# Optimization experiments

Hardware: AMD Instinct MI355X
Metric: run time of the kernel (lower is better)

## Reference

```python
import jax, jax.numpy as jnp
import numpy as np

N, E, G, D, C = 100000, 1600000, 128, 64, 10  # nodes, edges, graphs, feat dim, classes


def setup_inputs() -> dict:
    key = jax.random.key(0)
    ks = jax.random.split(key, 14)
    s = 0.05
    return {
        "x": jax.random.normal(ks[0], (N, D), jnp.float32),
        # edge update MLP: concat(h_src,h_dst) -> hidden -> message (dim D to allow u_mul_e)
        "We1": jax.random.normal(ks[1], (2 * D, D), jnp.float32) * s,
        "be1": jnp.zeros((D,), jnp.float32),
        "We2": jax.random.normal(ks[2], (D, D), jnp.float32) * s,
        "be2": jnp.zeros((D,), jnp.float32),
        # node update MLP (hidden_dim -> hidden_dim)
        "Wn": jax.random.normal(ks[3], (D, D), jnp.float32) * s,
        "bn": jnp.zeros((D,), jnp.float32),
        # attention-pooling gate Linear(hidden_dim, 1)
        "Wg": jax.random.normal(ks[4], (D, 1), jnp.float32) * s,
        "bg": jnp.zeros((1,), jnp.float32),
        # final classifier
        "Wfc": jax.random.normal(ks[5], (D, C), jnp.float32) * s,
        "bfc": jnp.zeros((C,), jnp.float32),
        # graph structure
        "src": jax.random.randint(ks[6], (E,), 0, N),
        "dst": jax.random.randint(ks[7], (E,), 0, N),
        "graph_ids": jnp.sort(jax.random.randint(ks[8], (N,), 0, G)),
    }


def reference(x, We1, be1, We2, be2, Wn, bn, Wg, bg, Wfc, bfc, src, dst, graph_ids):
    h = x  # [N, D]
    # apply_edges: edge MLP on (h_src, h_dst) -> message m per edge  [E, D]
    e_in = jnp.concatenate([h[src], h[dst]], axis=-1)  # [E, 2D]
    m = jax.nn.relu(e_in @ We1 + be1) @ We2 + be2
    # update_all: u_mul_e('h','m') then sum-reduce onto destination nodes
    h_neigh = jax.ops.segment_sum(h[src] * m, dst, num_segments=N)  # [N, D]
    # apply_nodes: node MLP
    h2 = jax.nn.relu(h_neigh @ Wn + bn)  # [N, D]
    # GlobalAttentionPooling: per-graph softmax over node gates, weighted sum
    gate = h2 @ Wg + bg  # [N, 1]
    gmax = jax.ops.segment_max(gate, graph_ids, num_segments=G)  # [G, 1]
    a = jnp.exp(gate - gmax[graph_ids])
    denom = jax.ops.segment_sum(a, graph_ids, num_segments=G)  # [G, 1]
    a = a / denom[graph_ids]
    pooled = jax.ops.segment_sum(a * h2, graph_ids, num_segments=G)  # [G, D]
    return pooled @ Wfc + bfc  # [G, C]
```

## Files before the change

kernel.cpp:

```cpp
#include <hip/hip_runtime.h>
#include <hip/hip_bf16.h>

#define D 64
#define BSH 6
#define BNODES 64
#define NBMAX 2048
#define EB 4096

typedef _Float16 f16;
typedef _Float16 f16x4 __attribute__((ext_vector_type(4)));
typedef _Float16 f16x8 __attribute__((ext_vector_type(8)));
typedef float f32x4 __attribute__((ext_vector_type(4)));

__device__ __forceinline__ int sw7(int m, int k) {
    return (m << 7) + (((k >> 3) ^ (m & 7)) << 3) + (k & 7);
}
__device__ __forceinline__ int sw6(int m, int k) {
    return (m << 6) + ((((k >> 3) ^ (m & 7)) & 7) << 3) + (k & 7);
}

__global__ __launch_bounds__(256) void bucket_hist(
    const int* __restrict__ dst, int* __restrict__ bhist, int E, int NB)
{
    __shared__ int lhist[NBMAX];
    int tid = threadIdx.x;
    for (int b = tid; b < NB; b += 256) lhist[b] = 0;
    __syncthreads();
    int base = blockIdx.x * EB;
#pragma unroll
    for (int r = 0; r < EB / 256; ++r) {
        int e = base + r * 256 + tid;
        if (e < E) atomicAdd(&lhist[dst[e] >> BSH], 1);
    }
    __syncthreads();
    for (int b = tid; b < NB; b += 256) {
        int v = lhist[b];
        if (v) atomicAdd(&bhist[b], v);
    }
}

__global__ __launch_bounds__(256) void bucket_scan(
    const int* __restrict__ bhist, int* __restrict__ boff,
    int* __restrict__ bcursor, int NB)
{
    __shared__ int lds[256];
    int tid = threadIdx.x;
    int chunk = (NB + 255) / 256;
    int b0 = tid * chunk;
    int b1 = min(b0 + chunk, NB);
    int s = 0;
    for (int b = b0; b < b1; ++b) s += bhist[b];
    lds[tid] = s;
    __syncthreads();
    for (int d2 = 1; d2 < 256; d2 <<= 1) {
        int v = (tid >= d2) ? lds[tid - d2] : 0;
        __syncthreads();
        lds[tid] += v;
        __syncthreads();
    }
    int run = (tid == 0) ? 0 : lds[tid - 1];
    for (int b = b0; b < b1; ++b) {
        boff[b] = run;
        bcursor[b] = run;
        run += bhist[b];
    }
    if (tid == 255) boff[NB] = lds[255];
}

__global__ __launch_bounds__(256) void bucket_fill(
    const int* __restrict__ dst, const int* __restrict__ src,
    int* __restrict__ bcursor, int2* __restrict__ eix, int E, int NB)
{
    __shared__ int lhist[NBMAX];
    __shared__ int lcur[NBMAX];
    int tid = threadIdx.x;
    for (int b = tid; b < NB; b += 256) lhist[b] = 0;
    __syncthreads();
    int base = blockIdx.x * EB;
    int dv[EB / 256];
#pragma unroll
    for (int r = 0; r < EB / 256; ++r) {
        int e = base + r * 256 + tid;
        dv[r] = (e < E) ? dst[e] : -1;
        if (dv[r] >= 0) atomicAdd(&lhist[dv[r] >> BSH], 1);
    }
    __syncthreads();
    for (int b = tid; b < NB; b += 256) {
        int v = lhist[b];
        lcur[b] = v ? atomicAdd(&bcursor[b], v) : 0;
    }
    __syncthreads();
#pragma unroll
    for (int r = 0; r < EB / 256; ++r) {
        int e = base + r * 256 + tid;
        if (dv[r] >= 0) {
            int p = atomicAdd(&lcur[dv[r] >> BSH], 1);
            eix[p] = make_int2(src[e], dv[r]);
        }
    }
}

__global__ __launch_bounds__(256) void bucket_sort(
    const int2* __restrict__ eix, const int* __restrict__ boff,
    int2* __restrict__ eix2, int NB)
{
    __shared__ int h64[BNODES];
    __shared__ int cur64[BNODES];
    int bk = blockIdx.x;
    int s = boff[bk], e = boff[bk + 1];
    int tid = threadIdx.x;
    int nbase = bk << BSH;

    if (tid < BNODES) h64[tid] = 0;
    __syncthreads();
    for (int i = s + tid; i < e; i += 256)
        atomicAdd(&h64[eix[i].y - nbase], 1);
    __syncthreads();
    if (tid < BNODES) {
        int v = h64[tid];
        int inc = v;
        for (int d2 = 1; d2 < BNODES; d2 <<= 1) {
            int t = __shfl_up(inc, d2);
            if (tid >= d2) inc += t;
        }
        cur64[tid] = inc - v;
    }
    __syncthreads();
    for (int i = s + tid; i < e; i += 256) {
        int2 ed = eix[i];
        int slot = atomicAdd(&cur64[ed.y - nbase], 1);
        eix2[s + slot] = ed;
    }
}

__global__ __launch_bounds__(256, 2) void edge_mfma_kernel(
    const float* __restrict__ x,
    const float* __restrict__ We1, const float* __restrict__ be1,
    const float* __restrict__ We2, const float* __restrict__ be2,
    const int2* __restrict__ eix,
    float* __restrict__ hneigh, int N, int E, int T)
{
    __shared__ __attribute__((aligned(16))) float XCs[4][16 * 68];
    __shared__ __attribute__((aligned(16))) f16   Hbs[4][16 * 64];
    __shared__ int edsts[4][16];

    const int tid  = threadIdx.x;
    const int w    = tid >> 6;
    const int lane = tid & 63;
    const int l15  = lane & 15;
    const int quad = lane >> 4;

    float* XC  = XCs[w];
    f16*   Hb  = Hbs[w];
    int*   edst = edsts[w];

    f16x8 wb1[4][4];
#pragma unroll
    for (int kt = 0; kt < 4; ++kt)
#pragma unroll
        for (int nf = 0; nf < 4; ++nf) {
            int n = nf * 16 + l15;
#pragma unroll
            for (int j = 0; j < 8; ++j)
                wb1[kt][nf][j] = (f16)We1[(kt * 32 + quad * 8 + j) * 64 + n];
        }
    f16x8 wb2[2][4];
#pragma unroll
    for (int kt = 0; kt < 2; ++kt)
#pragma unroll
        for (int nf = 0; nf < 4; ++nf) {
            int n = nf * 16 + l15;
#pragma unroll
            for (int j = 0; j < 8; ++j)
                wb2[kt][nf][j] = (f16)We2[(kt * 32 + quad * 8 + j) * 64 + n];
        }

    float b1v[4], b2v[4];
#pragma unroll
    for (int nf = 0; nf < 4; ++nf) {
        b1v[nf] = be1[nf * 16 + l15];
        b2v[nf] = be2[nf * 16 + l15];
    }

    const int wid = blockIdx.x * 4 + w;
    const int nw  = gridDim.x * 4;

    for (int tile = wid; tile < T; tile += nw) {
        const int e0 = tile * 16;

        int2 pe = eix[min(e0 + l15, E - 1)];
        const float* ps = x + (size_t)pe.x * D;
        const float* pd = x + (size_t)pe.y * D;
        float4 s0 = *(const float4*)(ps + quad * 8);
        float4 s1 = *(const float4*)(ps + quad * 8 + 4);
        float4 s2 = *(const float4*)(ps + 32 + quad * 8);
        float4 s3 = *(const float4*)(ps + 32 + quad * 8 + 4);
        float4 d0v = *(const float4*)(pd + quad * 8);
        float4 d1v = *(const float4*)(pd + quad * 8 + 4);
        float4 d2v = *(const float4*)(pd + 32 + quad * 8);
        float4 d3v = *(const float4*)(pd + 32 + quad * 8 + 4);

        int prevD = (e0 > 0)      ? eix[e0 - 1].y  : -2;
        int nextD = (e0 + 16 < E) ? eix[e0 + 16].y : -2;

        *(float4*)&XC[l15 * 68 + quad * 8]          = s0;
        *(float4*)&XC[l15 * 68 + quad * 8 + 4]      = s1;
        *(float4*)&XC[l15 * 68 + 32 + quad * 8]     = s2;
        *(float4*)&XC[l15 * 68 + 32 + quad * 8 + 4] = s3;
        if (quad == 0) edst[l15] = (e0 + l15 < E) ? pe.y : N;

        f16x8 ah[4];
        ah[0][0]=(f16)s0.x; ah[0][1]=(f16)s0.y; ah[0][2]=(f16)s0.z; ah[0][3]=(f16)s0.w;
        ah[0][4]=(f16)s1.x; ah[0][5]=(f16)s1.y; ah[0][6]=(f16)s1.z; ah[0][7]=(f16)s1.w;
        ah[1][0]=(f16)s2.x; ah[1][1]=(f16)s2.y; ah[1][2]=(f16)s2.z; ah[1][3]=(f16)s2.w;
        ah[1][4]=(f16)s3.x; ah[1][5]=(f16)s3.y; ah[1][6]=(f16)s3.z; ah[1][7]=(f16)s3.w;
        ah[2][0]=(f16)d0v.x; ah[2][1]=(f16)d0v.y; ah[2][2]=(f16)d0v.z; ah[2][3]=(f16)d0v.w;
        ah[2][4]=(f16)d1v.x; ah[2][5]=(f16)d1v.y; ah[2][6]=(f16)d1v.z; ah[2][7]=(f16)d1v.w;
        ah[3][0]=(f16)d2v.x; ah[3][1]=(f16)d2v.y; ah[3][2]=(f16)d2v.z; ah[3][3]=(f16)d2v.w;
        ah[3][4]=(f16)d3v.x; ah[3][5]=(f16)d3v.y; ah[3][6]=(f16)d3v.z; ah[3][7]=(f16)d3v.w;

        f32x4 acc[4] = {{0.f,0.f,0.f,0.f},{0.f,0.f,0.f,0.f},
                        {0.f,0.f,0.f,0.f},{0.f,0.f,0.f,0.f}};
#pragma unroll
        for (int kt = 0; kt < 4; ++kt)
#pragma unroll
            for (int nf = 0; nf < 4; ++nf)
                acc[nf] = __builtin_amdgcn_mfma_f32_16x16x32_f16(
                    ah[kt], wb1[kt][nf], acc[nf], 0, 0, 0);

#pragma unroll
        for (int nf = 0; nf < 4; ++nf)
#pragma unroll
            for (int i2 = 0; i2 < 4; ++i2)
                Hb[sw6(quad * 4 + i2, nf * 16 + l15)] =
                    (f16)fmaxf(acc[nf][i2] + b1v[nf], 0.f);

        f32x4 dd[4] = {{0.f,0.f,0.f,0.f},{0.f,0.f,0.f,0.f},
                       {0.f,0.f,0.f,0.f},{0.f,0.f,0.f,0.f}};
#pragma unroll
        for (int kt = 0; kt < 2; ++kt) {
            f16x8 ah2 = *(const f16x8*)&Hb[sw6(l15, kt * 32 + quad * 8)];
#pragma unroll
            for (int nf = 0; nf < 4; ++nf)
                dd[nf] = __builtin_amdgcn_mfma_f32_16x16x32_f16(
                    ah2, wb2[kt][nf], dd[nf], 0, 0, 0);
        }

#pragma unroll
        for (int nf = 0; nf < 4; ++nf)
#pragma unroll
            for (int i2 = 0; i2 < 4; ++i2) {
                int a = (quad * 4 + i2) * 68 + nf * 16 + l15;
                XC[a] = (dd[nf][i2] + b2v[nf]) * XC[a];
            }

        {
            int j = lane;
            float a = 0.f;
            int cur = edst[0];
            int runStart = 0;
#pragma unroll
            for (int ii = 0; ii < 16; ++ii) {
                a += XC[ii * 68 + j];
                int nxt = (ii < 15) ? edst[ii + 1] : -3;
                if (nxt != cur) {
                    bool firstRun = (runStart == 0);
                    bool lastRun = (ii == 15) || (nxt >= N);
                    bool complete = (!firstRun || prevD != cur) &&
                                    (!lastRun || nextD != cur);
                    if (complete) hneigh[(size_t)cur * D + j] = a;
                    else atomicAdd(&hneigh[(size_t)cur * D + j], a);
                    a = 0.f; cur = nxt; runStart = ii + 1;
                }
            }
        }
    }
}

__global__ __launch_bounds__(256, 4) void node_mfma_kernel(
    float* __restrict__ h,
    const float* __restrict__ Wn, const float* __restrict__ bn,
    const float* __restrict__ Wg, const float* __restrict__ bg,
    float* __restrict__ gate, int N, int T)
{
    __shared__ __attribute__((aligned(16))) f16 ANhi[64 * 64];
    __shared__ __attribute__((aligned(16))) f16 ANlo[64 * 64];

    const int tid = threadIdx.x;
    const int w = tid >> 6;
    const int lane = tid & 63;
    const int l15 = lane & 15;
    const int quad = lane >> 4;
    const int m0 = w * 16;

    f16x8 wn[2][4];
#pragma unroll
    for (int kt = 0; kt < 2; ++kt)
#pragma unroll
        for (int nf = 0; nf < 4; ++nf) {
            int n = nf * 16 + l15;
#pragma unroll
            for (int j = 0; j < 8; ++j)
                wn[kt][nf][j] = (f16)Wn[(kt * 32 + quad * 8 + j) * 64 + n];
        }

    float bnv[4], wgv[4];
#pragma unroll
    for (int nt = 0; nt < 4; ++nt) {
        bnv[nt] = bn[nt * 16 + l15];
        wgv[nt] = Wg[nt * 16 + l15];
    }
    const float bgv = bg[0];

    for (int tile = blockIdx.x; tile < T; tile += gridDim.x) {
        const int t0 = tile * 64;

        {
            int i = tid >> 2;
            int q = tid & 3;
            int node = min(t0 + i, N - 1);
            const float* p = h + (size_t)node * D + q * 16;
#pragma unroll
            for (int r = 0; r < 4; ++r) {
                float4 v = *(const float4*)(p + r * 4);
                int k = q * 16 + r * 4;
                f16x4 hv, lv;
                hv[0] = (f16)v.x; lv[0] = (f16)(v.x - (float)hv[0]);
                hv[1] = (f16)v.y; lv[1] = (f16)(v.y - (float)hv[1]);
                hv[2] = (f16)v.z; lv[2] = (f16)(v.z - (float)hv[2]);
                hv[3] = (f16)v.w; lv[3] = (f16)(v.w - (float)hv[3]);
                *(f16x4*)&ANhi[sw6(i, k)] = hv;
                *(f16x4*)&ANlo[sw6(i, k)] = lv;
            }
        }
        __syncthreads();

        f32x4 cacc[4] = {{0.f,0.f,0.f,0.f},{0.f,0.f,0.f,0.f},{0.f,0.f,0.f,0.f},{0.f,0.f,0.f,0.f}};
#pragma unroll
        for (int kt = 0; kt < 2; ++kt) {
            int k = kt * 32 + quad * 8;
            f16x8 ah = *(const f16x8*)&ANhi[sw6(m0 + l15, k)];
            f16x8 al = *(const f16x8*)&ANlo[sw6(m0 + l15, k)];
#pragma unroll
            for (int nf = 0; nf < 4; ++nf) {
                cacc[nf] = __builtin_amdgcn_mfma_f32_16x16x32_f16(ah, wn[kt][nf], cacc[nf], 0, 0, 0);
                cacc[nf] = __builtin_amdgcn_mfma_f32_16x16x32_f16(al, wn[kt][nf], cacc[nf], 0, 0, 0);
            }
        }
        __syncthreads();

        float gpart[4] = {0.f, 0.f, 0.f, 0.f};
#pragma unroll
        for (int nt = 0; nt < 4; ++nt) {
            int n = nt * 16 + l15;
#pragma unroll
            for (int i2 = 0; i2 < 4; ++i2) {
                int m = t0 + m0 + quad * 4 + i2;
                float v = fmaxf(cacc[nt][i2] + bnv[nt], 0.f);
                if (m < N) h[(size_t)m * D + n] = v;
                gpart[i2] += v * wgv[nt];
            }
        }
#pragma unroll
        for (int s = 1; s < 16; s <<= 1) {
#pragma unroll
            for (int i2 = 0; i2 < 4; ++i2) gpart[i2] += __shfl_xor(gpart[i2], s);
        }
        if (l15 == 0) {
#pragma unroll
            for (int i2 = 0; i2 < 4; ++i2) {
                int m = t0 + m0 + quad * 4 + i2;
                if (m < N) gate[m] = gpart[i2] + bgv;
            }
        }
    }
}

__global__ __launch_bounds__(256) void pool_kernel(
    const float* __restrict__ h2,
    const float* __restrict__ gate,
    const int* __restrict__ gid,
    const float* __restrict__ Wfc, const float* __restrict__ bfc,
    float* __restrict__ out, int N, int C)
{
    int g = blockIdx.x;
    int tid = threadIdx.x;

    int lo = 0, hi = N;
    while (lo < hi) { int mid = (lo + hi) >> 1; if (gid[mid] < g) lo = mid + 1; else hi = mid; }
    int s = lo;
    hi = N;
    while (lo < hi) { int mid = (lo + hi) >> 1; if (gid[mid] < g + 1) lo = mid + 1; else hi = mid; }
    int e = lo;

    __shared__ float red[256];
    __shared__ float accs[4][D];
    __shared__ float dens[4];

    float m = -INFINITY;
    for (int i = s + tid; i < e; i += 256) m = fmaxf(m, gate[i]);
    red[tid] = m;
    __syncthreads();
    for (int w = 128; w > 0; w >>= 1) {
        if (tid < w) red[tid] = fmaxf(red[tid], red[tid + w]);
        __syncthreads();
    }
    float gmax = red[0];
    __syncthreads();

    int f = tid & (D - 1);
    int grp = tid >> 6;
    float acc = 0.0f, den = 0.0f;
    for (int i = s + grp; i < e; i += 4) {
        float w = expf(gate[i] - gmax);
        acc += w * h2[(size_t)i * D + f];
        if (f == 0) den += w;
    }
    accs[grp][f] = acc;
    if (f == 0) dens[grp] = den;
    __syncthreads();

    if (tid < D) {
        float p = accs[0][tid] + accs[1][tid] + accs[2][tid] + accs[3][tid];
        float dn = dens[0] + dens[1] + dens[2] + dens[3];
        p = (e > s) ? (p / dn) : 0.0f;
        red[tid] = p;
    }
    __syncthreads();

    if (tid < C) {
        float o = bfc[tid];
#pragma unroll
        for (int k = 0; k < D; ++k) o += red[k] * Wfc[k * C + tid];
        out[g * C + tid] = o;
    }
}

extern "C" void kernel_launch(void* const* d_in, const int* in_sizes, int n_in,
                              void* d_out, int out_size, void* d_ws, size_t ws_size,
                              hipStream_t stream) {
    const float* x   = (const float*)d_in[0];
    const float* We1 = (const float*)d_in[1];
    const float* be1 = (const float*)d_in[2];
    const float* We2 = (const float*)d_in[3];
    const float* be2 = (const float*)d_in[4];
    const float* Wn  = (const float*)d_in[5];
    const float* bn  = (const float*)d_in[6];
    const float* Wg  = (const float*)d_in[7];
    const float* bg  = (const float*)d_in[8];
    const float* Wfc = (const float*)d_in[9];
    const float* bfc = (const float*)d_in[10];
    const int* src = (const int*)d_in[11];
    const int* dst = (const int*)d_in[12];
    const int* gid = (const int*)d_in[13];

    const int N = in_sizes[0] / D;
    const int E = in_sizes[11];
    const int C = 10;
    const int G = out_size / C;
    const int NB = (N + BNODES - 1) / BNODES;

    int2*  eix2   = (int2*)d_ws;
    int2*  eixA   = eix2 + E;
    float* hneigh = (float*)eixA;
    float* gate   = hneigh + (size_t)(N + 1) * D;
    int*   bhist  = (int*)(gate + N);
    int*   boff   = bhist + NB;
    int*   bcursor= boff + NB + 1;
    float* outp   = (float*)d_out;

    const int Bh = (E + EB - 1) / EB;
    const int Te = (E + 15) / 16;
    const int Tn = (N + 63) / 64;

    hipMemsetAsync(bhist, 0, (size_t)NB * sizeof(int), stream);

    bucket_hist<<<Bh, 256, 0, stream>>>(dst, bhist, E, NB);
    bucket_scan<<<1, 256, 0, stream>>>(bhist, boff, bcursor, NB);
    bucket_fill<<<Bh, 256, 0, stream>>>(dst, src, bcursor, eixA, E, NB);
    bucket_sort<<<NB, 256, 0, stream>>>(eixA, boff, eix2, NB);

    hipMemsetAsync(hneigh, 0, (size_t)(N + 1) * D * sizeof(float), stream);

    edge_mfma_kernel<<<512, 256, 0, stream>>>(x, We1, be1, We2, be2,
                                              eix2, hneigh, N, E, Te);
    node_mfma_kernel<<<1024, 256, 0, stream>>>(hneigh, Wn, bn, Wg, bg, gate, N, Tn);
    pool_kernel<<<G, 256, 0, stream>>>(hneigh, gate, gid, Wfc, bfc, outp, N, C);
}
```

Baseline: 391.2 us.

## Process two 16-edge subtiles per wave and prefetch next tile's edge indices

Each wave in the edge kernel now handles 32 edges per iteration as two interleaved 16-row MFMA subtiles, doubling the independent gathers and MFMA chains in flight. The edge index pairs for the next tile are loaded one iteration ahead to hide the dependent index-to-feature load latency. Segment reduction runs over 32 rows, so fewer partial runs hit atomics at tile boundaries. This raises register and LDS use per wave, which can reduce occupancy under the 2-blocks-per-CU launch bound.

```diff
diff --git a/kernel.cpp b/kernel.cpp
--- a/kernel.cpp
+++ b/kernel.cpp
@@ -12,9 +12,6 @@
 typedef _Float16 f16x8 __attribute__((ext_vector_type(8)));
 typedef float f32x4 __attribute__((ext_vector_type(4)));
 
-__device__ __forceinline__ int sw7(int m, int k) {
-    return (m << 7) + (((k >> 3) ^ (m & 7)) << 3) + (k & 7);
-}
 __device__ __forceinline__ int sw6(int m, int k) {
     return (m << 6) + ((((k >> 3) ^ (m & 7)) & 7) << 3) + (k & 7);
 }
@@ -140,9 +137,9 @@
     const int2* __restrict__ eix,
     float* __restrict__ hneigh, int N, int E, int T)
 {
-    __shared__ __attribute__((aligned(16))) float XCs[4][16 * 68];
-    __shared__ __attribute__((aligned(16))) f16   Hbs[4][16 * 64];
-    __shared__ int edsts[4][16];
+    __shared__ __attribute__((aligned(16))) float XCs[4][32 * 68];
+    __shared__ __attribute__((aligned(16))) f16   Hbs[4][32 * 64];
+    __shared__ int edsts[4][32];
 
     const int tid  = threadIdx.x;
     const int w    = tid >> 6;
@@ -185,73 +182,120 @@
     const int wid = blockIdx.x * 4 + w;
     const int nw  = gridDim.x * 4;
 
+    int2 peA = eix[min(wid * 32 + l15, E - 1)];
+    int2 peB = eix[min(wid * 32 + 16 + l15, E - 1)];
+
     for (int tile = wid; tile < T; tile += nw) {
-        const int e0 = tile * 16;
-
-        int2 pe = eix[min(e0 + l15, E - 1)];
-        const float* ps = x + (size_t)pe.x * D;
-        const float* pd = x + (size_t)pe.y * D;
-        float4 s0 = *(const float4*)(ps + quad * 8);
-        float4 s1 = *(const float4*)(ps + quad * 8 + 4);
-        float4 s2 = *(const float4*)(ps + 32 + quad * 8);
-        float4 s3 = *(const float4*)(ps + 32 + quad * 8 + 4);
-        float4 d0v = *(const float4*)(pd + quad * 8);
-        float4 d1v = *(const float4*)(pd + quad * 8 + 4);
-        float4 d2v = *(const float4*)(pd + 32 + quad * 8);
-        float4 d3v = *(const float4*)(pd + 32 + quad * 8 + 4);
+        const int e0 = tile * 32;
+
+        const float* psA = x + (size_t)peA.x * D;
+        const float* pdA = x + (size_t)peA.y * D;
+        const float* psB = x + (size_t)peB.x * D;
+        const float* pdB = x + (size_t)peB.y * D;
+        float4 sA0 = *(const float4*)(psA + quad * 8);
+        float4 sA1 = *(const float4*)(psA + quad * 8 + 4);
+        float4 sA2 = *(const float4*)(psA + 32 + quad * 8);
+        float4 sA3 = *(const float4*)(psA + 32 + quad * 8 + 4);
+        float4 dA0 = *(const float4*)(pdA + quad * 8);
+        float4 dA1 = *(const float4*)(pdA + quad * 8 + 4);
+        float4 dA2 = *(const float4*)(pdA + 32 + quad * 8);
+        float4 dA3 = *(const float4*)(pdA + 32 + quad * 8 + 4);
+        float4 sB0 = *(const float4*)(psB + quad * 8);
+        float4 sB1 = *(const float4*)(psB + quad * 8 + 4);
+        float4 sB2 = *(const float4*)(psB + 32 + quad * 8);
+        float4 sB3 = *(const float4*)(psB + 32 + quad * 8 + 4);
+        float4 dB0 = *(const float4*)(pdB + quad * 8);
+        float4 dB1 = *(const float4*)(pdB + quad * 8 + 4);
+        float4 dB2 = *(const float4*)(pdB + 32 + quad * 8);
+        float4 dB3 = *(const float4*)(pdB + 32 + quad * 8 + 4);
+
+        int tn = tile + nw;
+        int2 peA_n = eix[min(tn * 32 + l15, E - 1)];
+        int2 peB_n = eix[min(tn * 32 + 16 + l15, E - 1)];
 
         int prevD = (e0 > 0)      ? eix[e0 - 1].y  : -2;
-        int nextD = (e0 + 16 < E) ? eix[e0 + 16].y : -2;
-
-        *(float4*)&XC[l15 * 68 + quad * 8]          = s0;
-        *(float4*)&XC[l15 * 68 + quad * 8 + 4]      = s1;
-        *(float4*)&XC[l15 * 68 + 32 + quad * 8]     = s2;
-        *(float4*)&XC[l15 * 68 + 32 + quad * 8 + 4] = s3;
-        if (quad == 0) edst[l15] = (e0 + l15 < E) ? pe.y : N;
-
-        f16x8 ah[4];
-        ah[0][0]=(f16)s0.x; ah[0][1]=(f16)s0.y; ah[0][2]=(f16)s0.z; ah[0][3]=(f16)s0.w;
-        ah[0][4]=(f16)s1.x; ah[0][5]=(f16)s1.y; ah[0][6]=(f16)s1.z; ah[0][7]=(f16)s1.w;
-        ah[1][0]=(f16)s2.x; ah[1][1]=(f16)s2.y; ah[1][2]=(f16)s2.z; ah[1][3]=(f16)s2.w;
-        ah[1][4]=(f16)s3.x; ah[1][5]=(f16)s3.y; ah[1][6]=(f16)s3.z; ah[1][7]=(f16)s3.w;
-        ah[2][0]=(f16)d0v.x; ah[2][1]=(f16)d0v.y; ah[2][2]=(f16)d0v.z; ah[2][3]=(f16)d0v.w;
-        ah[2][4]=(f16)d1v.x; ah[2][5]=(f16)d1v.y; ah[2][6]=(f16)d1v.z; ah[2][7]=(f16)d1v.w;
-        ah[3][0]=(f16)d2v.x; ah[3][1]=(f16)d2v.y; ah[3][2]=(f16)d2v.z; ah[3][3]=(f16)d2v.w;
-        ah[3][4]=(f16)d3v.x; ah[3][5]=(f16)d3v.y; ah[3][6]=(f16)d3v.z; ah[3][7]=(f16)d3v.w;
-
-        f32x4 acc[4] = {{0.f,0.f,0.f,0.f},{0.f,0.f,0.f,0.f},
+        int nextD = (e0 + 32 < E) ? eix[e0 + 32].y : -2;
+
+        *(float4*)&XC[l15 * 68 + quad * 8]               = sA0;
+        *(float4*)&XC[l15 * 68 + quad * 8 + 4]           = sA1;
+        *(float4*)&XC[l15 * 68 + 32 + quad * 8]          = sA2;
+        *(float4*)&XC[l15 * 68 + 32 + quad * 8 + 4]      = sA3;
+        *(float4*)&XC[(16 + l15) * 68 + quad * 8]          = sB0;
+        *(float4*)&XC[(16 + l15) * 68 + quad * 8 + 4]      = sB1;
+        *(float4*)&XC[(16 + l15) * 68 + 32 + quad * 8]     = sB2;
+        *(float4*)&XC[(16 + l15) * 68 + 32 + quad * 8 + 4] = sB3;
+        if (quad == 0) {
+            edst[l15]      = (e0 + l15 < E)      ? peA.y : N;
+            edst[16 + l15] = (e0 + 16 + l15 < E) ? peB.y : N;
+        }
+
+        f16x8 ahA[4], ahB[4];
+        ahA[0][0]=(f16)sA0.x; ahA[0][1]=(f16)sA0.y; ahA[0][2]=(f16)sA0.z; ahA[0][3]=(f16)sA0.w;
+        ahA[0][4]=(f16)sA1.x; ahA[0][5]=(f16)sA1.y; ahA[0][6]=(f16)sA1.z; ahA[0][7]=(f16)sA1.w;
+        ahA[1][0]=(f16)sA2.x; ahA[1][1]=(f16)sA2.y; ahA[1][2]=(f16)sA2.z; ahA[1][3]=(f16)sA2.w;
+        ahA[1][4]=(f16)sA3.x; ahA[1][5]=(f16)sA3.y; ahA[1][6]=(f16)sA3.z; ahA[1][7]=(f16)sA3.w;
+        ahA[2][0]=(f16)dA0.x; ahA[2][1]=(f16)dA0.y; ahA[2][2]=(f16)dA0.z; ahA[2][3]=(f16)dA0.w;
+        ahA[2][4]=(f16)dA1.x; ahA[2][5]=(f16)dA1.y; ahA[2][6]=(f16)dA1.z; ahA[2][7]=(f16)dA1.w;
+        ahA[3][0]=(f16)dA2.x; ahA[3][1]=(f16)dA2.y; ahA[3][2]=(f16)dA2.z; ahA[3][3]=(f16)dA2.w;
+        ahA[3][4]=(f16)dA3.x; ahA[3][5]=(f16)dA3.y; ahA[3][6]=(f16)dA3.z; ahA[3][7]=(f16)dA3.w;
+        ahB[0][0]=(f16)sB0.x; ahB[0][1]=(f16)sB0.y; ahB[0][2]=(f16)sB0.z; ahB[0][3]=(f16)sB0.w;
+        ahB[0][4]=(f16)sB1.x; ahB[0][5]=(f16)sB1.y; ahB[0][6]=(f16)sB1.z; ahB[0][7]=(f16)sB1.w;
+        ahB[1][0]=(f16)sB2.x; ahB[1][1]=(f16)sB2.y; ahB[1][2]=(f16)sB2.z; ahB[1][3]=(f16)sB2.w;
+        ahB[1][4]=(f16)sB3.x; ahB[1][5]=(f16)sB3.y; ahB[1][6]=(f16)sB3.z; ahB[1][7]=(f16)sB3.w;
+        ahB[2][0]=(f16)dB0.x; ahB[2][1]=(f16)dB0.y; ahB[2][2]=(f16)dB0.z; ahB[2][3]=(f16)dB0.w;
+        ahB[2][4]=(f16)dB1.x; ahB[2][5]=(f16)dB1.y; ahB[2][6]=(f16)dB1.z; ahB[2][7]=(f16)dB1.w;
+        ahB[3][0]=(f16)dB2.x; ahB[3][1]=(f16)dB2.y; ahB[3][2]=(f16)dB2.z; ahB[3][3]=(f16)dB2.w;
+        ahB[3][4]=(f16)dB3.x; ahB[3][5]=(f16)dB3.y; ahB[3][6]=(f16)dB3.z; ahB[3][7]=(f16)dB3.w;
+
+        f32x4 accA[4] = {{0.f,0.f,0.f,0.f},{0.f,0.f,0.f,0.f},
+                         {0.f,0.f,0.f,0.f},{0.f,0.f,0.f,0.f}};
+        f32x4 accB[4] = {{0.f,0.f,0.f,0.f},{0.f,0.f,0.f,0.f},
+                         {0.f,0.f,0.f,0.f},{0.f,0.f,0.f,0.f}};
+#pragma unroll
+        for (int kt = 0; kt < 4; ++kt)
+#pragma unroll
+            for (int nf = 0; nf < 4; ++nf) {
+                accA[nf] = __builtin_amdgcn_mfma_f32_16x16x32_f16(
+                    ahA[kt], wb1[kt][nf], accA[nf], 0, 0, 0);
+                accB[nf] = __builtin_amdgcn_mfma_f32_16x16x32_f16(
+                    ahB[kt], wb1[kt][nf], accB[nf], 0, 0, 0);
+            }
+
+#pragma unroll
+        for (int nf = 0; nf < 4; ++nf)
+#pragma unroll
+            for (int i2 = 0; i2 < 4; ++i2) {
+                Hb[sw6(quad * 4 + i2, nf * 16 + l15)] =
+                    (f16)fmaxf(accA[nf][i2] + b1v[nf], 0.f);
+                Hb[sw6(16 + quad * 4 + i2, nf * 16 + l15)] =
+                    (f16)fmaxf(accB[nf][i2] + b1v[nf], 0.f);
+            }
+
+        f32x4 ddA[4] = {{0.f,0.f,0.f,0.f},{0.f,0.f,0.f,0.f},
                         {0.f,0.f,0.f,0.f},{0.f,0.f,0.f,0.f}};
-#pragma unroll
-        for (int kt = 0; kt < 4; ++kt)
-#pragma unroll
-            for (int nf = 0; nf < 4; ++nf)
-                acc[nf] = __builtin_amdgcn_mfma_f32_16x16x32_f16(
-                    ah[kt], wb1[kt][nf], acc[nf], 0, 0, 0);
+        f32x4 ddB[4] = {{0.f,0.f,0.f,0.f},{0.f,0.f,0.f,0.f},
+                        {0.f,0.f,0.f,0.f},{0.f,0.f,0.f,0.f}};
+#pragma unroll
+        for (int kt = 0; kt < 2; ++kt) {
+            f16x8 a2A = *(const f16x8*)&Hb[sw6(l15,      kt * 32 + quad * 8)];
+            f16x8 a2B = *(const f16x8*)&Hb[sw6(16 + l15, kt * 32 + quad * 8)];
+#pragma unroll
+            for (int nf = 0; nf < 4; ++nf) {
+                ddA[nf] = __builtin_amdgcn_mfma_f32_16x16x32_f16(
+                    a2A, wb2[kt][nf], ddA[nf], 0, 0, 0);
+                ddB[nf] = __builtin_amdgcn_mfma_f32_16x16x32_f16(
+                    a2B, wb2[kt][nf], ddB[nf], 0, 0, 0);
+            }
+        }
 
 #pragma unroll
         for (int nf = 0; nf < 4; ++nf)
 #pragma unroll
-            for (int i2 = 0; i2 < 4; ++i2)
-                Hb[sw6(quad * 4 + i2, nf * 16 + l15)] =
-                    (f16)fmaxf(acc[nf][i2] + b1v[nf], 0.f);
-
-        f32x4 dd[4] = {{0.f,0.f,0.f,0.f},{0.f,0.f,0.f,0.f},
-                       {0.f,0.f,0.f,0.f},{0.f,0.f,0.f,0.f}};
-#pragma unroll
-        for (int kt = 0; kt < 2; ++kt) {
-            f16x8 ah2 = *(const f16x8*)&Hb[sw6(l15, kt * 32 + quad * 8)];
-#pragma unroll
-            for (int nf = 0; nf < 4; ++nf)
-                dd[nf] = __builtin_amdgcn_mfma_f32_16x16x32_f16(
-                    ah2, wb2[kt][nf], dd[nf], 0, 0, 0);
-        }
-
-#pragma unroll
-        for (int nf = 0; nf < 4; ++nf)
-#pragma unroll
             for (int i2 = 0; i2 < 4; ++i2) {
-                int a = (quad * 4 + i2) * 68 + nf * 16 + l15;
-                XC[a] = (dd[nf][i2] + b2v[nf]) * XC[a];
+                int aA = (quad * 4 + i2) * 68 + nf * 16 + l15;
+                int aB = (16 + quad * 4 + i2) * 68 + nf * 16 + l15;
+                XC[aA] = (ddA[nf][i2] + b2v[nf]) * XC[aA];
+                XC[aB] = (ddB[nf][i2] + b2v[nf]) * XC[aB];
             }
 
         {
@@ -260,12 +304,12 @@
             int cur = edst[0];
             int runStart = 0;
 #pragma unroll
-            for (int ii = 0; ii < 16; ++ii) {
+            for (int ii = 0; ii < 32; ++ii) {
                 a += XC[ii * 68 + j];
-                int nxt = (ii < 15) ? edst[ii + 1] : -3;
+                int nxt = (ii < 31) ? edst[ii + 1] : -3;
                 if (nxt != cur) {
                     bool firstRun = (runStart == 0);
-                    bool lastRun = (ii == 15) || (nxt >= N);
+                    bool lastRun = (ii == 31) || (nxt >= N);
                     bool complete = (!firstRun || prevD != cur) &&
                                     (!lastRun || nextD != cur);
                     if (complete) hneigh[(size_t)cur * D + j] = a;
@@ -274,6 +318,8 @@
                 }
             }
         }
+
+        peA = peA_n; peB = peB_n;
     }
 }
 
@@ -470,7 +516,7 @@
     float* outp   = (float*)d_out;
 
     const int Bh = (E + EB - 1) / EB;
-    const int Te = (E + 15) / 16;
+    const int Te = (E + 31) / 32;
     const int Tn = (N + 63) / 64;
 
     hipMemsetAsync(bhist, 0, (size_t)NB * sizeof(int), stream);
```

Result: no change. 387.1 us (-1.0%).
